# Optimization experiments

Measured on AMD Instinct MI355X. Metric: run time of the kernel, lower is better.

Reference implementation:

```python
import jax, jax.numpy as jnp
import numpy as np

B, T, D, U = 64, 4096, 256, 64

def setup_inputs() -> dict:
    key = jax.random.key(0)
    k1, k2, k3 = jax.random.split(key, 3)
    inputs = jax.random.normal(k1, (B, T, D), dtype=jnp.float32)
    # glorot_uniform init for W (D,U) and u (U,1); zeros bias
    limW = float(np.sqrt(6.0 / (D + U)))
    W = jax.random.uniform(k2, (D, U), minval=-limW, maxval=limW, dtype=jnp.float32)
    limu = float(np.sqrt(6.0 / (U + 1)))
    u = jax.random.uniform(k3, (U, 1), minval=-limu, maxval=limu, dtype=jnp.float32)
    b = jnp.zeros((U,), dtype=jnp.float32)
    return {"inputs": inputs, "W": W, "b": b, "u": u}

def reference(inputs, W, b, u):
    # score: [B,T,U] = tanh(inputs @ W + b)
    score = jnp.tanh(jnp.einsum('btd,du->btu', inputs, W) + b)
    # logits: [B,T,1]; softmax over time axis (axis=1)
    logits = jnp.einsum('btu,uo->bto', score, u)
    attention_weights = jax.nn.softmax(logits, axis=1)
    # weighted sum over time -> [B,D]
    context = jnp.sum(inputs * attention_weights, axis=1)
    return (context, attention_weights)
```

## Files before the change

kernel.cpp:

```cpp
#include <hip/hip_runtime.h>
#include <math.h>

#define B_ 64
#define T_ 4096
#define D_ 256
#define U_ 64
#define TM 128
#define TC 256

typedef float f32x4 __attribute__((ext_vector_type(4)));
typedef short bf16x8 __attribute__((ext_vector_type(8)));

__device__ __forceinline__ unsigned short f2bf_rne(float f) {
    unsigned u = __float_as_uint(f);
    unsigned r = u + 0x7fffu + ((u >> 16) & 1u);
    return (unsigned short)(r >> 16);
}
__device__ __forceinline__ float bfbits2f(unsigned short s) {
    return __uint_as_float(((unsigned)s) << 16);
}

__global__ __launch_bounds__(256) void wprep_kernel(
    const float* __restrict__ W, unsigned short* __restrict__ whi,
    unsigned short* __restrict__ wlo)
{
    int fi = blockIdx.x * 256 + threadIdx.x;
    int j    = fi & 7;
    int lane = (fi >> 3) & 63;
    int tile = fi >> 9;
    int nt = tile & 3, ks = tile >> 2;
    int k = ks * 32 + (lane >> 4) * 8 + j;
    int n = nt * 16 + (lane & 15);
    float w = W[k * U_ + n];
    unsigned short hi = f2bf_rne(w);
    unsigned short lo = f2bf_rne(w - bfbits2f(hi));
    whi[fi] = hi;
    wlo[fi] = lo;
}

__global__ __launch_bounds__(256) void logits_mfma(
    const float* __restrict__ x, const unsigned short* __restrict__ whi,
    const unsigned short* __restrict__ wlo, const float* __restrict__ bias,
    const float* __restrict__ uvec, float* __restrict__ wts,
    unsigned short* __restrict__ xbf, float* __restrict__ Zp)
{
    __shared__ unsigned short Bh[16384];
    __shared__ unsigned short Bl[16384];
    __shared__ float zred[4];

    int tid = threadIdx.x;
    {
        const uint4* sh = (const uint4*)whi;
        const uint4* sl = (const uint4*)wlo;
        uint4* dh = (uint4*)Bh;
        uint4* dl = (uint4*)Bl;
#pragma unroll
        for (int i = 0; i < 8; ++i) {
            dh[tid + i * 256] = sh[tid + i * 256];
            dl[tid + i * 256] = sl[tid + i * 256];
        }
    }
    __syncthreads();

    int lane = tid & 63, wid = tid >> 6;
    int q = lane >> 4, r = lane & 15;
    size_t R0 = (size_t)blockIdx.x * TM;
    size_t row0 = R0 + wid * 16 + r;
    size_t row1 = row0 + 64;
    const float* x0 = x + row0 * D_;
    const float* x1 = x + row1 * D_;
    unsigned short* xo0 = xbf + row0 * D_;
    unsigned short* xo1 = xbf + row1 * D_;

    f32x4 acc0[4], acc1[4];
#pragma unroll
    for (int nt = 0; nt < 4; ++nt) {
        acc0[nt] = (f32x4){0.f, 0.f, 0.f, 0.f};
        acc1[nt] = (f32x4){0.f, 0.f, 0.f, 0.f};
    }

    const bf16x8* BhV = (const bf16x8*)Bh;
    const bf16x8* BlV = (const bf16x8*)Bl;

#pragma unroll 4
    for (int ks = 0; ks < 8; ++ks) {
        int k0 = ks * 32 + q * 8;
        float4 va0 = *(const float4*)(x0 + k0);
        float4 vb0 = *(const float4*)(x0 + k0 + 4);
        float4 va1 = *(const float4*)(x1 + k0);
        float4 vb1 = *(const float4*)(x1 + k0 + 4);
        float f0[8] = {va0.x, va0.y, va0.z, va0.w, vb0.x, vb0.y, vb0.z, vb0.w};
        float f1[8] = {va1.x, va1.y, va1.z, va1.w, vb1.x, vb1.y, vb1.z, vb1.w};
        union { bf16x8 v; unsigned short s[8]; uint4 u; } h0, l0, h1, l1;
#pragma unroll
        for (int j = 0; j < 8; ++j) {
            unsigned short a = f2bf_rne(f0[j]);
            h0.s[j] = a;
            l0.s[j] = f2bf_rne(f0[j] - bfbits2f(a));
            unsigned short c = f2bf_rne(f1[j]);
            h1.s[j] = c;
            l1.s[j] = f2bf_rne(f1[j] - bfbits2f(c));
        }
        *(uint4*)(xo0 + k0) = h0.u;
        *(uint4*)(xo1 + k0) = h1.u;
#pragma unroll
        for (int nt = 0; nt < 4; ++nt) {
            bf16x8 bh = BhV[(ks * 4 + nt) * 64 + lane];
            bf16x8 bl = BlV[(ks * 4 + nt) * 64 + lane];
            acc0[nt] = __builtin_amdgcn_mfma_f32_16x16x32_bf16(h0.v, bh, acc0[nt], 0, 0, 0);
            acc0[nt] = __builtin_amdgcn_mfma_f32_16x16x32_bf16(h0.v, bl, acc0[nt], 0, 0, 0);
            acc0[nt] = __builtin_amdgcn_mfma_f32_16x16x32_bf16(l0.v, bh, acc0[nt], 0, 0, 0);
            acc1[nt] = __builtin_amdgcn_mfma_f32_16x16x32_bf16(h1.v, bh, acc1[nt], 0, 0, 0);
            acc1[nt] = __builtin_amdgcn_mfma_f32_16x16x32_bf16(h1.v, bl, acc1[nt], 0, 0, 0);
            acc1[nt] = __builtin_amdgcn_mfma_f32_16x16x32_bf16(l1.v, bh, acc1[nt], 0, 0, 0);
        }
    }

    float zsum = 0.f;
#pragma unroll
    for (int s = 0; s < 2; ++s) {
        f32x4* A = s ? acc1 : acc0;
        float p0 = 0.f, p1 = 0.f, p2 = 0.f, p3 = 0.f;
#pragma unroll
        for (int nt = 0; nt < 4; ++nt) {
            int col = nt * 16 + r;
            float bv = bias[col], uv = uvec[col];
            float s0 = A[nt][0] + bv, s1 = A[nt][1] + bv,
                  s2 = A[nt][2] + bv, s3 = A[nt][3] + bv;
            p0 = fmaf(1.f - 2.f / (__expf(2.f * s0) + 1.f), uv, p0);
            p1 = fmaf(1.f - 2.f / (__expf(2.f * s1) + 1.f), uv, p1);
            p2 = fmaf(1.f - 2.f / (__expf(2.f * s2) + 1.f), uv, p2);
            p3 = fmaf(1.f - 2.f / (__expf(2.f * s3) + 1.f), uv, p3);
        }
#pragma unroll
        for (int off = 1; off < 16; off <<= 1) {
            p0 += __shfl_xor(p0, off, 64);
            p1 += __shfl_xor(p1, off, 64);
            p2 += __shfl_xor(p2, off, 64);
            p3 += __shfl_xor(p3, off, 64);
        }
        float e0 = __expf(p0), e1 = __expf(p1), e2 = __expf(p2), e3 = __expf(p3);
        if (r == 0) {
            float4 o = {e0, e1, e2, e3};
            *(float4*)(wts + R0 + s * 64 + wid * 16 + q * 4) = o;
        }
        zsum += (e0 + e1) + (e2 + e3);
    }
    zsum += __shfl_xor(zsum, 16, 64);
    zsum += __shfl_xor(zsum, 32, 64);
    if (lane == 0) zred[wid] = zsum;
    __syncthreads();
    if (tid == 0) Zp[blockIdx.x] = (zred[0] + zred[1]) + (zred[2] + zred[3]);
}

__global__ __launch_bounds__(256) void context_kernel(
    const unsigned short* __restrict__ xbf, float* __restrict__ wts,
    const float* __restrict__ Zp, float* __restrict__ ctx)
{
    int b = blockIdx.y;
    int t0 = blockIdx.x * TC;
    int tid = threadIdx.x;
    int colg = tid & 31, ph = tid >> 5;

    float Z = 0.f;
#pragma unroll
    for (int i = 0; i < T_ / TM; ++i) Z += Zp[b * (T_ / TM) + i];
    float invZ = 1.f / Z;

    __shared__ float wsh[TC];
    float e = wts[(size_t)b * T_ + t0 + tid];
    wsh[tid] = e;
    wts[(size_t)b * T_ + t0 + tid] = e * invZ;
    __syncthreads();

    const unsigned short* xb = xbf + ((size_t)b * T_ + t0) * D_;
    float acc[8];
#pragma unroll
    for (int j = 0; j < 8; ++j) acc[j] = 0.f;

#pragma unroll 4
    for (int i = 0; i < TC; i += 8) {
        int row = i + ph;
        float w = wsh[row];
        union { uint4 u; unsigned short s[8]; } v;
        v.u = *(const uint4*)(xb + (size_t)row * D_ + colg * 8);
#pragma unroll
        for (int j = 0; j < 8; ++j)
            acc[j] = fmaf(w, bfbits2f(v.s[j]), acc[j]);
    }

    __shared__ float red[8 * 256];
#pragma unroll
    for (int j = 0; j < 8; ++j) red[ph * 256 + colg * 8 + j] = acc[j];
    __syncthreads();
    float ssum = 0.f;
#pragma unroll
    for (int p = 0; p < 8; ++p) ssum += red[p * 256 + tid];
    atomicAdd(&ctx[b * D_ + tid], ssum * invZ);
}

extern "C" void kernel_launch(void* const* d_in, const int* in_sizes, int n_in,
                              void* d_out, int out_size, void* d_ws, size_t ws_size,
                              hipStream_t stream) {
    const float* x    = (const float*)d_in[0];
    const float* W    = (const float*)d_in[1];
    const float* bias = (const float*)d_in[2];
    const float* uvec = (const float*)d_in[3];

    float* out = (float*)d_out;
    float* ctx = out;
    float* wts = out + B_ * D_;

    unsigned short* whi = (unsigned short*)d_ws;
    unsigned short* wlo = whi + D_ * U_;
    unsigned short* xbf = wlo + D_ * U_;
    float* Zp = (float*)(xbf + (size_t)B_ * T_ * D_);

    hipMemsetAsync(ctx, 0, B_ * D_ * sizeof(float), stream);

    wprep_kernel<<<D_ * U_ / 256, 256, 0, stream>>>(W, whi, wlo);
    logits_mfma<<<(B_ * T_) / TM, 256, 0, stream>>>(x, whi, wlo, bias, uvec, wts, xbf, Zp);
    context_kernel<<<dim3(T_ / TC, B_), 256, 0, stream>>>(xbf, wts, Zp, ctx);
}
```

Measured before the change: 434.5 us.

## Fuse context accumulation into logits kernel using LDS-staged bf16 rows

The logits kernel now keeps its bf16-converted input tile in shared memory and computes the unnormalized weighted context partial sum directly, atomically accumulating into a workspace buffer. A small finalize kernel then applies 1/Z to both the context and the attention weights. This removes the round trip of writing and re-reading a bf16 copy of the whole input (about 128 MB each way) through global memory. W tiles are now read straight from global/L2 instead of being staged in LDS. The larger LDS footprint (about 76 KB per block) may lower occupancy.

```diff
diff --git a/kernel.cpp b/kernel.cpp
--- a/kernel.cpp
+++ b/kernel.cpp
@@ -6,7 +6,7 @@
 #define D_ 256
 #define U_ 64
 #define TM 128
-#define TC 256
+#define XSTRIDE 264
 
 typedef float f32x4 __attribute__((ext_vector_type(4)));
 typedef short bf16x8 __attribute__((ext_vector_type(8)));
@@ -38,39 +38,26 @@
     wlo[fi] = lo;
 }
 
-__global__ __launch_bounds__(256) void logits_mfma(
+__global__ __launch_bounds__(256) void fused_main(
     const float* __restrict__ x, const unsigned short* __restrict__ whi,
     const unsigned short* __restrict__ wlo, const float* __restrict__ bias,
     const float* __restrict__ uvec, float* __restrict__ wts,
-    unsigned short* __restrict__ xbf, float* __restrict__ Zp)
+    float* __restrict__ Zp, float* __restrict__ accZ)
 {
-    __shared__ unsigned short Bh[16384];
-    __shared__ unsigned short Bl[16384];
+    __shared__ unsigned short Xh[TM * XSTRIDE];
+    __shared__ float esh[TM];
+    __shared__ float red[8 * 256];
     __shared__ float zred[4];
 
     int tid = threadIdx.x;
-    {
-        const uint4* sh = (const uint4*)whi;
-        const uint4* sl = (const uint4*)wlo;
-        uint4* dh = (uint4*)Bh;
-        uint4* dl = (uint4*)Bl;
-#pragma unroll
-        for (int i = 0; i < 8; ++i) {
-            dh[tid + i * 256] = sh[tid + i * 256];
-            dl[tid + i * 256] = sl[tid + i * 256];
-        }
-    }
-    __syncthreads();
-
     int lane = tid & 63, wid = tid >> 6;
     int q = lane >> 4, r = lane & 15;
+
     size_t R0 = (size_t)blockIdx.x * TM;
-    size_t row0 = R0 + wid * 16 + r;
-    size_t row1 = row0 + 64;
-    const float* x0 = x + row0 * D_;
-    const float* x1 = x + row1 * D_;
-    unsigned short* xo0 = xbf + row0 * D_;
-    unsigned short* xo1 = xbf + row1 * D_;
+    int lrow0 = wid * 16 + r;
+    int lrow1 = lrow0 + 64;
+    const float* x0 = x + (R0 + lrow0) * D_;
+    const float* x1 = x + (R0 + lrow1) * D_;
 
     f32x4 acc0[4], acc1[4];
 #pragma unroll
@@ -79,8 +66,8 @@
         acc1[nt] = (f32x4){0.f, 0.f, 0.f, 0.f};
     }
 
-    const bf16x8* BhV = (const bf16x8*)Bh;
-    const bf16x8* BlV = (const bf16x8*)Bl;
+    const bf16x8* BhV = (const bf16x8*)whi;
+    const bf16x8* BlV = (const bf16x8*)wlo;
 
 #pragma unroll 4
     for (int ks = 0; ks < 8; ++ks) {
@@ -101,8 +88,8 @@
             h1.s[j] = c;
             l1.s[j] = f2bf_rne(f1[j] - bfbits2f(c));
         }
-        *(uint4*)(xo0 + k0) = h0.u;
-        *(uint4*)(xo1 + k0) = h1.u;
+        *(uint4*)(&Xh[lrow0 * XSTRIDE + k0]) = h0.u;
+        *(uint4*)(&Xh[lrow1 * XSTRIDE + k0]) = h1.u;
 #pragma unroll
         for (int nt = 0; nt < 4; ++nt) {
             bf16x8 bh = BhV[(ks * 4 + nt) * 64 + lane];
@@ -142,7 +129,9 @@
         float e0 = __expf(p0), e1 = __expf(p1), e2 = __expf(p2), e3 = __expf(p3);
         if (r == 0) {
             float4 o = {e0, e1, e2, e3};
-            *(float4*)(wts + R0 + s * 64 + wid * 16 + q * 4) = o;
+            int lr = s * 64 + wid * 16 + q * 4;
+            *(float4*)(wts + R0 + lr) = o;
+            *(float4*)(&esh[lr]) = o;
         }
         zsum += (e0 + e1) + (e2 + e3);
     }
@@ -151,52 +140,52 @@
     if (lane == 0) zred[wid] = zsum;
     __syncthreads();
     if (tid == 0) Zp[blockIdx.x] = (zred[0] + zred[1]) + (zred[2] + zred[3]);
-}
-
-__global__ __launch_bounds__(256) void context_kernel(
-    const unsigned short* __restrict__ xbf, float* __restrict__ wts,
-    const float* __restrict__ Zp, float* __restrict__ ctx)
+
+    int colg = tid & 31, ph = tid >> 5;
+    float pacc[8];
+#pragma unroll
+    for (int j = 0; j < 8; ++j) pacc[j] = 0.f;
+#pragma unroll 4
+    for (int i = 0; i < TM; i += 8) {
+        int row = i + ph;
+        float w = esh[row];
+        union { uint4 u; unsigned short s[8]; } v;
+        v.u = *(const uint4*)(&Xh[row * XSTRIDE + colg * 8]);
+#pragma unroll
+        for (int j = 0; j < 8; ++j)
+            pacc[j] = fmaf(w, bfbits2f(v.s[j]), pacc[j]);
+    }
+    float4* redv = (float4*)(&red[ph * 256 + colg * 8]);
+    redv[0] = (float4){pacc[0], pacc[1], pacc[2], pacc[3]};
+    redv[1] = (float4){pacc[4], pacc[5], pacc[6], pacc[7]};
+    __syncthreads();
+    float ssum = 0.f;
+#pragma unroll
+    for (int p = 0; p < 8; ++p) ssum += red[p * 256 + tid];
+    int b = blockIdx.x >> 5;
+    atomicAdd(&accZ[b * D_ + tid], ssum);
+}
+
+__global__ __launch_bounds__(256) void finalize_kernel(
+    float* __restrict__ wts, const float* __restrict__ Zp,
+    const float* __restrict__ accZ, float* __restrict__ ctx)
 {
-    int b = blockIdx.y;
-    int t0 = blockIdx.x * TC;
+    int b = blockIdx.x;
     int tid = threadIdx.x;
-    int colg = tid & 31, ph = tid >> 5;
-
     float Z = 0.f;
 #pragma unroll
     for (int i = 0; i < T_ / TM; ++i) Z += Zp[b * (T_ / TM) + i];
     float invZ = 1.f / Z;
 
-    __shared__ float wsh[TC];
-    float e = wts[(size_t)b * T_ + t0 + tid];
-    wsh[tid] = e;
-    wts[(size_t)b * T_ + t0 + tid] = e * invZ;
-    __syncthreads();
-
-    const unsigned short* xb = xbf + ((size_t)b * T_ + t0) * D_;
-    float acc[8];
-#pragma unroll
-    for (int j = 0; j < 8; ++j) acc[j] = 0.f;
-
-#pragma unroll 4
-    for (int i = 0; i < TC; i += 8) {
-        int row = i + ph;
-        float w = wsh[row];
-        union { uint4 u; unsigned short s[8]; } v;
-        v.u = *(const uint4*)(xb + (size_t)row * D_ + colg * 8);
-#pragma unroll
-        for (int j = 0; j < 8; ++j)
-            acc[j] = fmaf(w, bfbits2f(v.s[j]), acc[j]);
-    }
-
-    __shared__ float red[8 * 256];
-#pragma unroll
-    for (int j = 0; j < 8; ++j) red[ph * 256 + colg * 8 + j] = acc[j];
-    __syncthreads();
-    float ssum = 0.f;
-#pragma unroll
-    for (int p = 0; p < 8; ++p) ssum += red[p * 256 + tid];
-    atomicAdd(&ctx[b * D_ + tid], ssum * invZ);
+    ctx[b * D_ + tid] = accZ[b * D_ + tid] * invZ;
+
+    float4* wp = (float4*)(wts + (size_t)b * T_);
+#pragma unroll
+    for (int i = 0; i < T_ / 4 / 256; ++i) {
+        float4 v = wp[tid + i * 256];
+        v.x *= invZ; v.y *= invZ; v.z *= invZ; v.w *= invZ;
+        wp[tid + i * 256] = v;
+    }
 }
 
 extern "C" void kernel_launch(void* const* d_in, const int* in_sizes, int n_in,
@@ -213,12 +202,12 @@
 
     unsigned short* whi = (unsigned short*)d_ws;
     unsigned short* wlo = whi + D_ * U_;
-    unsigned short* xbf = wlo + D_ * U_;
-    float* Zp = (float*)(xbf + (size_t)B_ * T_ * D_);
-
-    hipMemsetAsync(ctx, 0, B_ * D_ * sizeof(float), stream);
+    float* Zp   = (float*)(wlo + D_ * U_);
+    float* accZ = Zp + (B_ * T_) / TM;
+
+    hipMemsetAsync(accZ, 0, B_ * D_ * sizeof(float), stream);
 
     wprep_kernel<<<D_ * U_ / 256, 256, 0, stream>>>(W, whi, wlo);
-    logits_mfma<<<(B_ * T_) / TM, 256, 0, stream>>>(x, whi, wlo, bias, uvec, wts, xbf, Zp);
-    context_kernel<<<dim3(T_ / TC, B_), 256, 0, stream>>>(xbf, wts, Zp, ctx);
-}
+    fused_main<<<(B_ * T_) / TM, 256, 0, stream>>>(x, whi, wlo, bias, uvec, wts, Zp, accZ);
+    finalize_kernel<<<B_, 256, 0, stream>>>(wts, Zp, accZ, ctx);
+}
```

New measurement: 435.9 us. About the same (+0.3%).
